# Optimization experiments

Measured on AMD Instinct MI355X. Metric: run time of the kernel, lower is better.

## Reference

```python
import jax, jax.numpy as jnp
import numpy as np

EPS = 1e-10

def _quantize_one(x, codebook):
    # x: [B, T, D]; codebook: [K, D]
    B, T, D = x.shape
    K = codebook.shape[0]
    flat = x.reshape(-1, D)  # [N, D]
    # squared euclidean distance (argmin of this == argmax of -dist in torch code)
    dist = (jnp.sum(flat * flat, axis=-1, keepdims=True)
            - 2.0 * flat @ codebook.T
            + jnp.sum(codebook * codebook, axis=-1))  # [N, K]
    ind = jnp.argmin(dist, axis=-1)  # [N]
    q = codebook[ind].reshape(B, T, D)
    # commitment loss: mse(quantize.detach(), x) * commitment(=1.0)
    loss = jnp.mean((jax.lax.stop_gradient(q) - x) ** 2)
    # straight-through estimator
    q_st = x + jax.lax.stop_gradient(q - x)
    # perplexity from one-hot encodings
    counts = jnp.zeros((K,), dtype=x.dtype).at[ind].add(1.0)
    avg_probs = counts / ind.shape[0]
    perplexity = jnp.exp(-jnp.sum(avg_probs * jnp.log(avg_probs + EPS)))
    return q_st, loss, perplexity

def setup_inputs() -> dict:
    key = jax.random.key(0)
    k1, k2 = jax.random.split(key)
    z = jax.random.normal(k1, (16, 64, 4096), dtype=jnp.float32)
    codebooks = jax.random.normal(k2, (8, 1024, 64), dtype=jnp.float32)
    return {"z": z, "codebooks": codebooks}

def reference(z, codebooks):
    # z: [B, code_dim, T] -> transpose(2,1) -> [B, T, code_dim]
    x = jnp.transpose(z, (0, 2, 1))

    def step(carry, cb):
        residual, quantized_out = carry
        q, loss, perp = _quantize_one(residual, cb)
        return (residual - q, quantized_out + q), (loss, perp)

    (_, quantized_out), (losses, perplexities) = jax.lax.scan(
        step, (x, jnp.zeros_like(x)), codebooks)
    zq = jnp.transpose(quantized_out, (0, 2, 1))  # back to [B, code_dim, T]
    return zq, losses, perplexities
```

## Files before the change

### kernel.cpp

```cpp
#include <hip/hip_runtime.h>

#define S      8
#define K      1024
#define D      64
#define NVEC   65536
#define NW     2048
#define NELEM  4194304.0f
#define EPSQ   1e-10f
#define DELTA  0.005f

typedef __attribute__((ext_vector_type(8))) short  short8;
typedef __attribute__((ext_vector_type(4))) float  float4v;

static __device__ inline unsigned short f2bf(float f) {
    unsigned int u = __float_as_uint(f);
    u = (u + 0x7FFFu + ((u >> 16) & 1u)) >> 16;
    return (unsigned short)u;
}
static __device__ inline float bf2f(unsigned short h) {
    return __uint_as_float(((unsigned int)h) << 16);
}

__global__ void rvq_prep(const float* __restrict__ cb,
                         unsigned short* __restrict__ cbi,
                         float* __restrict__ c2, unsigned* __restrict__ cnt) {
    int i = blockIdx.x * blockDim.x + threadIdx.x;
    if (i < S * K) {
        const float* row = cb + (size_t)i * D;
        float a0 = 0.f, a1 = 0.f, a2 = 0.f, a3 = 0.f;
#pragma unroll
        for (int d = 0; d < D; d += 4) {
            a0 = fmaf(row[d+0], row[d+0], a0);
            a1 = fmaf(row[d+1], row[d+1], a1);
            a2 = fmaf(row[d+2], row[d+2], a2);
            a3 = fmaf(row[d+3], row[d+3], a3);
        }
        c2[i] = (a0 + a1) + (a2 + a3);
        cnt[i] = 0u;
    }
    int s  = i >> 12;
    int tau = (i >> 6) & 63;
    int l  = i & 63;
    int m  = l & 15, qq = l >> 4;
    const float* row = cb + (size_t)(s * K + tau * 16 + m) * D;
    short8 h0h, h0l, h1h, h1l;
#pragma unroll
    for (int e = 0; e < 8; ++e) {
        float x = -2.0f * row[qq * 8 + e];
        unsigned short h = f2bf(x);
        h0h[e] = (short)h; h0l[e] = (short)f2bf(x - bf2f(h));
        float y = -2.0f * row[32 + qq * 8 + e];
        unsigned short g = f2bf(y);
        h1h[e] = (short)g; h1l[e] = (short)f2bf(y - bf2f(g));
    }
    unsigned short* rec = cbi + (size_t)(s * 64 + tau) * 2048 + l * 8;
    *(short8*)(rec +    0) = h0h;
    *(short8*)(rec +  512) = h1h;
    *(short8*)(rec + 1024) = h0l;
    *(short8*)(rec + 1536) = h1l;
}

__global__ __launch_bounds__(64, 2)
void rvq_main(const float* __restrict__ z, const float* __restrict__ cbf,
              const unsigned short* __restrict__ cbi,
              const float* __restrict__ c2, float* __restrict__ zq,
              float* __restrict__ lossp, unsigned* __restrict__ cnt) {
    const int lane = threadIdx.x;
    const int m    = lane & 15;
    const int q    = lane >> 4;
    const int wid  = blockIdx.x;
    const int vbase = wid * 32;
    const int b    = vbase >> 12;
    const int ta   = (vbase & 4095) + m;
    const int tb   = ta + 16;
    const size_t zrow = ((size_t)(b * 64)) << 12;
    const int lo16 = lane * 16;
    const int lom  = m * 4;

    __shared__ float rsp[32][65];

#pragma unroll
    for (int i = 0; i < 8; ++i) {
        rsp[m][q*8+i]         = z[zrow + ((size_t)(q*8+i)    << 12) + ta];
        rsp[m][32+q*8+i]      = z[zrow + ((size_t)(32+q*8+i) << 12) + ta];
        rsp[16+m][q*8+i]      = z[zrow + ((size_t)(q*8+i)    << 12) + tb];
        rsp[16+m][32+q*8+i]   = z[zrow + ((size_t)(32+q*8+i) << 12) + tb];
    }

#define LOADB(i) {                                                           \
        B##i##0 = *(const short8*)(tp + lo16);                               \
        B##i##1 = *(const short8*)(tp + lo16 + 1024);                        \
        B##i##2 = *(const short8*)(tp + lo16 + 2048);                        \
        B##i##3 = *(const short8*)(tp + lo16 + 3072);                        \
        cc##i   = *(const float*)(cp + lom);                                 \
        tp += 4096; cp += 64;                                                \
    }

#define MF(A,B,C) __builtin_amdgcn_mfma_f32_16x16x32_bf16(A,B,C,0,0,0)

#define COMPUTE(i, tt) {                                                     \
        float4v p0 = {cc##i, cc##i, cc##i, cc##i};                           \
        float4v p1 = {0.f, 0.f, 0.f, 0.f};                                   \
        float4v r0 = {cc##i, cc##i, cc##i, cc##i};                           \
        float4v r1 = {0.f, 0.f, 0.f, 0.f};                                   \
        __builtin_amdgcn_s_setprio(1);                                       \
        p0 = MF(xa0h, B##i##0, p0); r0 = MF(xb0h, B##i##0, r0);              \
        p1 = MF(xa1h, B##i##1, p1); r1 = MF(xb1h, B##i##1, r1);              \
        p0 = MF(xa0l, B##i##0, p0); r0 = MF(xb0l, B##i##0, r0);              \
        p1 = MF(xa1l, B##i##1, p1); r1 = MF(xb1l, B##i##1, r1);              \
        p0 = MF(xa0h, B##i##2, p0); r0 = MF(xb0h, B##i##2, r0);              \
        p1 = MF(xa1h, B##i##3, p1); r1 = MF(xb1h, B##i##3, r1);              \
        __builtin_amdgcn_s_setprio(0);                                       \
        const int ncol = (tt) * 16 + m;                                      \
        _Pragma("unroll")                                                    \
        for (int j = 0; j < 4; ++j) {                                        \
            float sa = p0[j] + p1[j];                                        \
            b2a[j] = __builtin_amdgcn_fmed3f(sa, b1a[j], b2a[j]);            \
            k1a[j] = (sa < b1a[j]) ? ncol : k1a[j];                          \
            b1a[j] = fminf(sa, b1a[j]);                                      \
            float sb = r0[j] + r1[j];                                        \
            b2b[j] = __builtin_amdgcn_fmed3f(sb, b1b[j], b2b[j]);            \
            k1b[j] = (sb < b1b[j]) ? ncol : k1b[j];                          \
            b1b[j] = fminf(sb, b1b[j]);                                      \
        }                                                                    \
    }

#pragma unroll 1
    for (int s = 0; s < S; ++s) {
        short8 xa0h, xa0l, xa1h, xa1l, xb0h, xb0l, xb1h, xb1l;
#pragma unroll
        for (int i = 0; i < 8; ++i) {
            unsigned short h; float v;
            v = rsp[m][q*8+i];        h = f2bf(v); xa0h[i] = (short)h; xa0l[i] = (short)f2bf(v - bf2f(h));
            v = rsp[m][32+q*8+i];     h = f2bf(v); xa1h[i] = (short)h; xa1l[i] = (short)f2bf(v - bf2f(h));
            v = rsp[16+m][q*8+i];     h = f2bf(v); xb0h[i] = (short)h; xb0l[i] = (short)f2bf(v - bf2f(h));
            v = rsp[16+m][32+q*8+i];  h = f2bf(v); xb1h[i] = (short)h; xb1l[i] = (short)f2bf(v - bf2f(h));
        }

        float b1a[4], b2a[4], b1b[4], b2b[4];
        int   k1a[4], k1b[4];
#pragma unroll
        for (int j = 0; j < 4; ++j) {
            b1a[j] = 3.4e38f; b2a[j] = 3.4e38f; k1a[j] = 0;
            b1b[j] = 3.4e38f; b2b[j] = 3.4e38f; k1b[j] = 0;
        }

        const float* c2s = c2 + s * K;
        const char*  tp  = (const char*)(cbi + (size_t)s * 131072);
        const char*  cp  = (const char*)c2s;

        short8 B00, B01, B02, B03, B10, B11, B12, B13;
        float  cc0, cc1;

        LOADB(0) LOADB(1)

#pragma unroll 1
        for (int it = 0; it < 31; ++it) {
            const int tau = it * 2;
            COMPUTE(0, tau + 0) LOADB(0)
            COMPUTE(1, tau + 1) LOADB(1)
        }
        COMPUTE(0, 62) COMPUTE(1, 63)

#pragma unroll
        for (int off = 1; off < 16; off <<= 1) {
#pragma unroll
            for (int j = 0; j < 4; ++j) {
                float o1 = __shfl_xor(b1a[j], off); int ok = __shfl_xor(k1a[j], off);
                float o2 = __shfl_xor(b2a[j], off);
                float n2 = fminf(fminf(b2a[j], o2), fmaxf(b1a[j], o1));
                bool tk = (o1 < b1a[j]) || (o1 == b1a[j] && ok < k1a[j]);
                k1a[j] = tk ? ok : k1a[j]; b1a[j] = fminf(b1a[j], o1); b2a[j] = n2;
                o1 = __shfl_xor(b1b[j], off); ok = __shfl_xor(k1b[j], off);
                o2 = __shfl_xor(b2b[j], off);
                n2 = fminf(fminf(b2b[j], o2), fmaxf(b1b[j], o1));
                tk = (o1 < b1b[j]) || (o1 == b1b[j] && ok < k1b[j]);
                k1b[j] = tk ? ok : k1b[j]; b1b[j] = fminf(b1b[j], o1); b2b[j] = n2;
            }
        }

        const float* cr0 = cbf + (size_t)s * 65536;
#define RESCUE(b1X, b2X, k1X, ROW)                                            \
        for (int j = 0; j < 4; ++j) {                                         \
            unsigned long long mask = __ballot(b2X[j] - b1X[j] < DELTA);      \
            while (mask) {                                                    \
                int lq = (int)(__builtin_ctzll(mask)) >> 4;                   \
                mask &= ~(0xFFFFULL << (lq * 16));                            \
                int mrow = lq * 4 + j;                                        \
                float bd = 3.4e38f; int bk = 0;                               \
                for (int cc = 0; cc < 16; ++cc) {                             \
                    int n = cc * 64 + lane;                                   \
                    const float* crow = cr0 + (size_t)n * 64;                 \
                    float dot = 0.f;                                          \
                    for (int d = 0; d < 64; ++d)                              \
                        dot = fmaf(rsp[(ROW) + mrow][d], crow[d], dot);       \
                    float sc = c2s[n] - 2.f * dot;                            \
                    if (sc < bd) { bd = sc; bk = n; }                         \
                }                                                             \
                for (int off = 1; off < 64; off <<= 1) {                      \
                    float ob = __shfl_xor(bd, off); int ok = __shfl_xor(bk, off); \
                    bool tk = (ob < bd) || (ob == bd && ok < bk);             \
                    bk = tk ? ok : bk; bd = fminf(bd, ob);                    \
                }                                                             \
                if (q == lq) k1X[j] = bk;                                     \
            }                                                                 \
        }
        RESCUE(b1a, b2a, k1a, 0)
        RESCUE(b1b, b2b, k1b, 16)
#undef RESCUE

        int mm = m & 3, src = (m >> 2) * 16;
        int wa0 = __shfl(k1a[0], src), wa1 = __shfl(k1a[1], src);
        int wa2 = __shfl(k1a[2], src), wa3 = __shfl(k1a[3], src);
        int bka = (mm == 0) ? wa0 : (mm == 1) ? wa1 : (mm == 2) ? wa2 : wa3;
        int wb0 = __shfl(k1b[0], src), wb1 = __shfl(k1b[1], src);
        int wb2 = __shfl(k1b[2], src), wb3 = __shfl(k1b[3], src);
        int bkb = (mm == 0) ? wb0 : (mm == 1) ? wb1 : (mm == 2) ? wb2 : wb3;

        const float* qa = cbf + (size_t)s * 65536 + (size_t)bka * 64;
        const float* qb = cbf + (size_t)s * 65536 + (size_t)bkb * 64;
        float ls = 0.f;
#pragma unroll
        for (int i = 0; i < 8; ++i) {
            float na = rsp[m][q*8+i]        - qa[q*8+i];
            float nb = rsp[m][32+q*8+i]     - qa[32+q*8+i];
            float nc = rsp[16+m][q*8+i]     - qb[q*8+i];
            float nd = rsp[16+m][32+q*8+i]  - qb[32+q*8+i];
            rsp[m][q*8+i] = na;        rsp[m][32+q*8+i] = nb;
            rsp[16+m][q*8+i] = nc;     rsp[16+m][32+q*8+i] = nd;
            ls = fmaf(na, na, ls); ls = fmaf(nb, nb, ls);
            ls = fmaf(nc, nc, ls); ls = fmaf(nd, nd, ls);
        }
#pragma unroll
        for (int off = 1; off < 64; off <<= 1) ls += __shfl_xor(ls, off);
        if (lane == 0) lossp[s * NW + wid] = ls;

        if (q == 0) {
            atomicAdd(&cnt[s * K + bka], 1u);
            atomicAdd(&cnt[s * K + bkb], 1u);
        }
    }
#undef LOADB
#undef COMPUTE
#undef MF

#pragma unroll
    for (int i = 0; i < 8; ++i) {
        size_t a0 = zrow + ((size_t)(q*8+i)    << 12) + ta;
        size_t a1 = zrow + ((size_t)(32+q*8+i) << 12) + ta;
        zq[a0] = z[a0] - rsp[m][q*8+i];
        zq[a1] = z[a1] - rsp[m][32+q*8+i];
        size_t a2 = zrow + ((size_t)(q*8+i)    << 12) + tb;
        size_t a3 = zrow + ((size_t)(32+q*8+i) << 12) + tb;
        zq[a2] = z[a2] - rsp[16+m][q*8+i];
        zq[a3] = z[a3] - rsp[16+m][32+q*8+i];
    }
}

__global__ void rvq_finalize(const float* __restrict__ lossp,
                             const unsigned* __restrict__ cnt,
                             float* __restrict__ out_loss,
                             float* __restrict__ out_perp) {
    const int s   = blockIdx.x;
    const int tid = threadIdx.x;
    float ent = 0.f, lsum = 0.f;
    for (int i = tid; i < K; i += 256) {
        float p = (float)cnt[s * K + i] * (1.0f / 65536.0f);
        ent += p * logf(p + EPSQ);
    }
    for (int i = tid; i < NW; i += 256) lsum += lossp[s * NW + i];
    __shared__ float redE[4], redL[4];
#pragma unroll
    for (int off = 32; off > 0; off >>= 1) {
        ent  += __shfl_down(ent, off);
        lsum += __shfl_down(lsum, off);
    }
    if ((tid & 63) == 0) { redE[tid >> 6] = ent; redL[tid >> 6] = lsum; }
    __syncthreads();
    if (tid == 0) {
        float te = redE[0] + redE[1] + redE[2] + redE[3];
        float tl = redL[0] + redL[1] + redL[2] + redL[3];
        out_perp[s] = expf(-te);
        out_loss[s] = tl * (1.0f / NELEM);
    }
}

extern "C" void kernel_launch(void* const* d_in, const int* in_sizes, int n_in,
                              void* d_out, int out_size, void* d_ws, size_t ws_size,
                              hipStream_t stream) {
    const float* z  = (const float*)d_in[0];
    const float* cb = (const float*)d_in[1];

    float* zq       = (float*)d_out;
    float* out_loss = zq + 4194304;
    float* out_perp = out_loss + 8;

    char* ws = (char*)d_ws;
    unsigned short* cbi = (unsigned short*)(ws);
    float*    c2    = (float*)(ws + 2097152);
    unsigned* cnt   = (unsigned*)(ws + 2129920);
    float*    lossp = (float*)(ws + 2162688);

    hipLaunchKernelGGL(rvq_prep,     dim3(128),  dim3(256), 0, stream, cb, cbi, c2, cnt);
    hipLaunchKernelGGL(rvq_main,     dim3(NW),   dim3(64),  0, stream, z, cb, cbi, c2, zq, lossp, cnt);
    hipLaunchKernelGGL(rvq_finalize, dim3(S),    dim3(256), 0, stream, lossp, cnt, out_loss, out_perp);
}
```

Measured before the change: 373.3 us.

## Split codebook scan across two waves per block with LDS merge of argmin

Each block now has two wavefronts. Each wave scans half of the 1024 codebook entries for the same 32 vectors, and the two partial top-2 results are merged through shared memory. The residual update, loss and count work is then split by vector half between the waves. This doubles the number of waves available to hide latency and halves the serial MFMA loop per wave. In exchange it adds __syncthreads barriers and LDS exchange every stage, and both waves still compute the full A-side MFMAs for both vector groups.

```diff
diff --git a/kernel.cpp b/kernel.cpp
--- a/kernel.cpp
+++ b/kernel.cpp
@@ -4,7 +4,8 @@
 #define K      1024
 #define D      64
 #define NVEC   65536
-#define NW     2048
+#define NBLK   2048
+#define NWL    4096
 #define NELEM  4194304.0f
 #define EPSQ   1e-10f
 #define DELTA  0.005f
@@ -60,32 +61,42 @@
     *(short8*)(rec + 1536) = h1l;
 }
 
-__global__ __launch_bounds__(64, 2)
+__global__ __launch_bounds__(128, 2)
 void rvq_main(const float* __restrict__ z, const float* __restrict__ cbf,
               const unsigned short* __restrict__ cbi,
               const float* __restrict__ c2, float* __restrict__ zq,
               float* __restrict__ lossp, unsigned* __restrict__ cnt) {
-    const int lane = threadIdx.x;
+    const int tid  = threadIdx.x;
+    const int lane = tid & 63;
+    const int w    = tid >> 6;
     const int m    = lane & 15;
     const int q    = lane >> 4;
-    const int wid  = blockIdx.x;
-    const int vbase = wid * 32;
+    const int bid  = blockIdx.x;
+    const int vbase = bid * 32;
     const int b    = vbase >> 12;
     const int ta   = (vbase & 4095) + m;
     const int tb   = ta + 16;
     const size_t zrow = ((size_t)(b * 64)) << 12;
     const int lo16 = lane * 16;
     const int lom  = m * 4;
+    const int tbase = w * 32;
 
     __shared__ float rsp[32][65];
+    __shared__ float lb1[2][2][16];
+    __shared__ float lb2[2][2][16];
+    __shared__ int   lk1[2][2][16];
 
 #pragma unroll
     for (int i = 0; i < 8; ++i) {
-        rsp[m][q*8+i]         = z[zrow + ((size_t)(q*8+i)    << 12) + ta];
-        rsp[m][32+q*8+i]      = z[zrow + ((size_t)(32+q*8+i) << 12) + ta];
-        rsp[16+m][q*8+i]      = z[zrow + ((size_t)(q*8+i)    << 12) + tb];
-        rsp[16+m][32+q*8+i]   = z[zrow + ((size_t)(32+q*8+i) << 12) + tb];
-    }
+        if (w == 0) {
+            rsp[m][q*8+i]       = z[zrow + ((size_t)(q*8+i)    << 12) + ta];
+            rsp[m][32+q*8+i]    = z[zrow + ((size_t)(32+q*8+i) << 12) + ta];
+        } else {
+            rsp[16+m][q*8+i]    = z[zrow + ((size_t)(q*8+i)    << 12) + tb];
+            rsp[16+m][32+q*8+i] = z[zrow + ((size_t)(32+q*8+i) << 12) + tb];
+        }
+    }
+    __syncthreads();
 
 #define LOADB(i) {                                                           \
         B##i##0 = *(const short8*)(tp + lo16);                               \
@@ -111,7 +122,7 @@
         p0 = MF(xa0h, B##i##2, p0); r0 = MF(xb0h, B##i##2, r0);              \
         p1 = MF(xa1h, B##i##3, p1); r1 = MF(xb1h, B##i##3, r1);              \
         __builtin_amdgcn_s_setprio(0);                                       \
-        const int ncol = (tt) * 16 + m;                                      \
+        const int ncol = (tbase + (tt)) * 16 + m;                            \
         _Pragma("unroll")                                                    \
         for (int j = 0; j < 4; ++j) {                                        \
             float sa = p0[j] + p1[j];                                        \
@@ -146,8 +157,8 @@
         }
 
         const float* c2s = c2 + s * K;
-        const char*  tp  = (const char*)(cbi + (size_t)s * 131072);
-        const char*  cp  = (const char*)c2s;
+        const char*  tp  = (const char*)(cbi + (size_t)s * 131072) + tbase * 4096;
+        const char*  cp  = (const char*)c2s + tbase * 64;
 
         short8 B00, B01, B02, B03, B10, B11, B12, B13;
         float  cc0, cc1;
@@ -155,12 +166,12 @@
         LOADB(0) LOADB(1)
 
 #pragma unroll 1
-        for (int it = 0; it < 31; ++it) {
+        for (int it = 0; it < 15; ++it) {
             const int tau = it * 2;
             COMPUTE(0, tau + 0) LOADB(0)
             COMPUTE(1, tau + 1) LOADB(1)
         }
-        COMPUTE(0, 62) COMPUTE(1, 63)
+        COMPUTE(0, 30) COMPUTE(1, 31)
 
 #pragma unroll
         for (int off = 1; off < 16; off <<= 1) {
@@ -173,6 +184,33 @@
                 k1a[j] = tk ? ok : k1a[j]; b1a[j] = fminf(b1a[j], o1); b2a[j] = n2;
                 o1 = __shfl_xor(b1b[j], off); ok = __shfl_xor(k1b[j], off);
                 o2 = __shfl_xor(b2b[j], off);
+                n2 = fminf(fminf(b2b[j], o2), fmaxf(b1b[j], o1));
+                tk = (o1 < b1b[j]) || (o1 == b1b[j] && ok < k1b[j]);
+                k1b[j] = tk ? ok : k1b[j]; b1b[j] = fminf(b1b[j], o1); b2b[j] = n2;
+            }
+        }
+
+        if (m == 0) {
+#pragma unroll
+            for (int j = 0; j < 4; ++j) {
+                lb1[w][0][q*4+j] = b1a[j]; lb2[w][0][q*4+j] = b2a[j];
+                lk1[w][0][q*4+j] = k1a[j];
+                lb1[w][1][q*4+j] = b1b[j]; lb2[w][1][q*4+j] = b2b[j];
+                lk1[w][1][q*4+j] = k1b[j];
+            }
+        }
+        __syncthreads();
+        {
+            int ow = w ^ 1;
+#pragma unroll
+            for (int j = 0; j < 4; ++j) {
+                float o1 = lb1[ow][0][q*4+j], o2 = lb2[ow][0][q*4+j];
+                int   ok = lk1[ow][0][q*4+j];
+                float n2 = fminf(fminf(b2a[j], o2), fmaxf(b1a[j], o1));
+                bool tk = (o1 < b1a[j]) || (o1 == b1a[j] && ok < k1a[j]);
+                k1a[j] = tk ? ok : k1a[j]; b1a[j] = fminf(b1a[j], o1); b2a[j] = n2;
+                o1 = lb1[ow][1][q*4+j]; o2 = lb2[ow][1][q*4+j];
+                ok = lk1[ow][1][q*4+j];
                 n2 = fminf(fminf(b2b[j], o2), fmaxf(b1b[j], o1));
                 tk = (o1 < b1b[j]) || (o1 == b1b[j] && ok < k1b[j]);
                 k1b[j] = tk ? ok : k1b[j]; b1b[j] = fminf(b1b[j], o1); b2b[j] = n2;
@@ -205,40 +243,44 @@
                 if (q == lq) k1X[j] = bk;                                     \
             }                                                                 \
         }
-        RESCUE(b1a, b2a, k1a, 0)
-        RESCUE(b1b, b2b, k1b, 16)
+        if (w == 0) { RESCUE(b1a, b2a, k1a, 0) }
+        else        { RESCUE(b1b, b2b, k1b, 16) }
 #undef RESCUE
 
         int mm = m & 3, src = (m >> 2) * 16;
-        int wa0 = __shfl(k1a[0], src), wa1 = __shfl(k1a[1], src);
-        int wa2 = __shfl(k1a[2], src), wa3 = __shfl(k1a[3], src);
-        int bka = (mm == 0) ? wa0 : (mm == 1) ? wa1 : (mm == 2) ? wa2 : wa3;
-        int wb0 = __shfl(k1b[0], src), wb1 = __shfl(k1b[1], src);
-        int wb2 = __shfl(k1b[2], src), wb3 = __shfl(k1b[3], src);
-        int bkb = (mm == 0) ? wb0 : (mm == 1) ? wb1 : (mm == 2) ? wb2 : wb3;
-
-        const float* qa = cbf + (size_t)s * 65536 + (size_t)bka * 64;
-        const float* qb = cbf + (size_t)s * 65536 + (size_t)bkb * 64;
         float ls = 0.f;
-#pragma unroll
-        for (int i = 0; i < 8; ++i) {
-            float na = rsp[m][q*8+i]        - qa[q*8+i];
-            float nb = rsp[m][32+q*8+i]     - qa[32+q*8+i];
-            float nc = rsp[16+m][q*8+i]     - qb[q*8+i];
-            float nd = rsp[16+m][32+q*8+i]  - qb[32+q*8+i];
-            rsp[m][q*8+i] = na;        rsp[m][32+q*8+i] = nb;
-            rsp[16+m][q*8+i] = nc;     rsp[16+m][32+q*8+i] = nd;
-            ls = fmaf(na, na, ls); ls = fmaf(nb, nb, ls);
-            ls = fmaf(nc, nc, ls); ls = fmaf(nd, nd, ls);
+        if (w == 0) {
+            int wa0 = __shfl(k1a[0], src), wa1 = __shfl(k1a[1], src);
+            int wa2 = __shfl(k1a[2], src), wa3 = __shfl(k1a[3], src);
+            int bka = (mm == 0) ? wa0 : (mm == 1) ? wa1 : (mm == 2) ? wa2 : wa3;
+            const float* qa = cbf + (size_t)s * 65536 + (size_t)bka * 64;
+#pragma unroll
+            for (int i = 0; i < 8; ++i) {
+                float na = rsp[m][q*8+i]    - qa[q*8+i];
+                float nb = rsp[m][32+q*8+i] - qa[32+q*8+i];
+                rsp[m][q*8+i] = na;  rsp[m][32+q*8+i] = nb;
+                ls = fmaf(na, na, ls); ls = fmaf(nb, nb, ls);
+            }
+            if (q == 0) atomicAdd(&cnt[s * K + bka], 1u);
+        } else {
+            int wb0 = __shfl(k1b[0], src), wb1 = __shfl(k1b[1], src);
+            int wb2 = __shfl(k1b[2], src), wb3 = __shfl(k1b[3], src);
+            int bkb = (mm == 0) ? wb0 : (mm == 1) ? wb1 : (mm == 2) ? wb2 : wb3;
+            const float* qb = cbf + (size_t)s * 65536 + (size_t)bkb * 64;
+#pragma unroll
+            for (int i = 0; i < 8; ++i) {
+                float nc = rsp[16+m][q*8+i]    - qb[q*8+i];
+                float nd = rsp[16+m][32+q*8+i] - qb[32+q*8+i];
+                rsp[16+m][q*8+i] = nc;  rsp[16+m][32+q*8+i] = nd;
+                ls = fmaf(nc, nc, ls); ls = fmaf(nd, nd, ls);
+            }
+            if (q == 0) atomicAdd(&cnt[s * K + bkb], 1u);
         }
 #pragma unroll
         for (int off = 1; off < 64; off <<= 1) ls += __shfl_xor(ls, off);
-        if (lane == 0) lossp[s * NW + wid] = ls;
-
-        if (q == 0) {
-            atomicAdd(&cnt[s * K + bka], 1u);
-            atomicAdd(&cnt[s * K + bkb], 1u);
-        }
+        if (lane == 0) lossp[s * NWL + bid * 2 + w] = ls;
+
+        __syncthreads();
     }
 #undef LOADB
 #undef COMPUTE
@@ -246,14 +288,17 @@
 
 #pragma unroll
     for (int i = 0; i < 8; ++i) {
-        size_t a0 = zrow + ((size_t)(q*8+i)    << 12) + ta;
-        size_t a1 = zrow + ((size_t)(32+q*8+i) << 12) + ta;
-        zq[a0] = z[a0] - rsp[m][q*8+i];
-        zq[a1] = z[a1] - rsp[m][32+q*8+i];
-        size_t a2 = zrow + ((size_t)(q*8+i)    << 12) + tb;
-        size_t a3 = zrow + ((size_t)(32+q*8+i) << 12) + tb;
-        zq[a2] = z[a2] - rsp[16+m][q*8+i];
-        zq[a3] = z[a3] - rsp[16+m][32+q*8+i];
+        if (w == 0) {
+            size_t a0 = zrow + ((size_t)(q*8+i)    << 12) + ta;
+            size_t a1 = zrow + ((size_t)(32+q*8+i) << 12) + ta;
+            zq[a0] = z[a0] - rsp[m][q*8+i];
+            zq[a1] = z[a1] - rsp[m][32+q*8+i];
+        } else {
+            size_t a2 = zrow + ((size_t)(q*8+i)    << 12) + tb;
+            size_t a3 = zrow + ((size_t)(32+q*8+i) << 12) + tb;
+            zq[a2] = z[a2] - rsp[16+m][q*8+i];
+            zq[a3] = z[a3] - rsp[16+m][32+q*8+i];
+        }
     }
 }
 
@@ -268,7 +313,7 @@
         float p = (float)cnt[s * K + i] * (1.0f / 65536.0f);
         ent += p * logf(p + EPSQ);
     }
-    for (int i = tid; i < NW; i += 256) lsum += lossp[s * NW + i];
+    for (int i = tid; i < NWL; i += 256) lsum += lossp[s * NWL + i];
     __shared__ float redE[4], redL[4];
 #pragma unroll
     for (int off = 32; off > 0; off >>= 1) {
@@ -302,6 +347,6 @@
     float*    lossp = (float*)(ws + 2162688);
 
     hipLaunchKernelGGL(rvq_prep,     dim3(128),  dim3(256), 0, stream, cb, cbi, c2, cnt);
-    hipLaunchKernelGGL(rvq_main,     dim3(NW),   dim3(64),  0, stream, z, cb, cbi, c2, zq, lossp, cnt);
+    hipLaunchKernelGGL(rvq_main,     dim3(NBLK), dim3(128), 0, stream, z, cb, cbi, c2, zq, lossp, cnt);
     hipLaunchKernelGGL(rvq_finalize, dim3(S),    dim3(256), 0, stream, lossp, cnt, out_loss, out_perp);
 }
```

New measurement: 401.1 us. 1.07x slower.
